# Kernel optimization log

Measured on AMD Instinct MI355X. Metric: run time of the kernel, lower is better.

Reference implementation:

```python
import jax, jax.numpy as jnp
import numpy as np

STATE_DIM = 128
NUM_STATES = 16
BATCH = 16384


def setup_inputs() -> dict:
    key = jax.random.key(0)
    k1, k2, k3, k4 = jax.random.split(key, 4)
    x = jax.random.normal(k1, (BATCH, STATE_DIM), dtype=jnp.float32)
    state_idx = jax.random.randint(k2, (BATCH,), 0, NUM_STATES)
    A_all = jax.random.normal(k3, (NUM_STATES, STATE_DIM, STATE_DIM), dtype=jnp.float32)
    C_all = jax.random.normal(k4, (NUM_STATES, STATE_DIM, STATE_DIM), dtype=jnp.float32)
    return {"x": x, "state_idx": state_idx, "A_all": A_all, "C_all": C_all}


def reference(x, state_idx, A_all, C_all):
    # Per-sample expert matrix gather: [B, D, D]
    Ag = A_all[state_idx]
    Cg = C_all[state_idx]
    # state = relu(x @ A_i) per sample, batched via einsum
    state = jax.nn.relu(jnp.einsum('bd,bde->be', x, Ag))
    # observation = state @ C_i
    out = jnp.einsum('be,bef->bf', state, Cg)
    return out
```

## Files before the change

### kernel.cpp

```cpp
#include <hip/hip_runtime.h>

#define D 128
#define NS 16
#define BATCH 16384
#define TILE 64
#define CHUNK 512
#define NCH (BATCH / CHUNK)

typedef __attribute__((ext_vector_type(8))) short short8;
typedef __attribute__((ext_vector_type(4))) float f32x4;

__device__ __forceinline__ unsigned short f2bf(float f) {
  unsigned u = __builtin_bit_cast(unsigned, f);
  u += 0x7FFFu + ((u >> 16) & 1u);
  return (unsigned short)(u >> 16);
}

__global__ __launch_bounds__(256, 2) void ssm_fused(
    const float* __restrict__ x,
    const int* __restrict__ sidx,
    const float* __restrict__ A_all,
    const float* __restrict__ C_all,
    float* __restrict__ out) {
  __shared__ __align__(16) char smemW[D * 136 * 2];
  unsigned short (*Ws)[136] = (unsigned short (*)[136])smemW;
  float (*T)[129] = (float (*)[129])smemW;
  __shared__ unsigned short Xs[TILE][136];
  __shared__ unsigned short Hs[TILE][136];
  __shared__ int rowlist[CHUNK];
  __shared__ int wcnt[8];

  const int s = blockIdx.y;
  const int c0 = blockIdx.x * CHUNK;
  const int tid = threadIdx.x;
  const int lane = tid & 63, w = tid >> 6;
  const int l15 = lane & 15, quad = lane >> 4;
  const int wr = w & 1, wc = w >> 1;

  const int v0 = sidx[c0 + tid];
  const int v1 = sidx[c0 + 256 + tid];
  const unsigned long long lanelt = (1ull << lane) - 1ull;
  const unsigned long long m0 = __ballot(v0 == s);
  const unsigned long long m1 = __ballot(v1 == s);
  if (lane == 0) { wcnt[w] = (int)__popcll(m0); wcnt[4 + w] = (int)__popcll(m1); }
  __syncthreads();
  int pre0 = 0, pre1 = 0, tot0 = 0, cnt = 0;
#pragma unroll
  for (int ww = 0; ww < 4; ww++) {
    if (ww < w) { pre0 += wcnt[ww]; pre1 += wcnt[4 + ww]; }
    tot0 += wcnt[ww];
    cnt += wcnt[ww] + wcnt[4 + ww];
  }
  if (v0 == s) rowlist[pre0 + (int)__popcll(m0 & lanelt)] = c0 + tid;
  if (v1 == s) rowlist[tot0 + pre1 + (int)__popcll(m1 & lanelt)] = c0 + 256 + tid;
  if (cnt == 0) return;

  uint4 atr[8], ctr[8];
  {
    const float* __restrict__ srcA = A_all + (size_t)s * D * D;
    const float* __restrict__ srcC = C_all + (size_t)s * D * D;
    const int ecol = (tid & 7) * 4;
    const int drow = tid >> 3;
#pragma unroll
    for (int mat = 0; mat < 2; mat++) {
      const float* __restrict__ src = mat ? srcC : srcA;
#pragma unroll
      for (int sl = 0; sl < 4; sl++) {
        const int e0 = sl * 32;
        __syncthreads();
#pragma unroll
        for (int i = 0; i < 4; i++) {
          const int d = drow + 32 * i;
          const float4 v = *(const float4*)(src + (size_t)d * D + e0 + ecol);
          T[ecol + 0][d] = v.x;
          T[ecol + 1][d] = v.y;
          T[ecol + 2][d] = v.z;
          T[ecol + 3][d] = v.w;
        }
        __syncthreads();
#pragma unroll
        for (int ii = 0; ii < 2; ii++) {
          const int c = (2 * sl + ii) * 256 + tid;
          const int e = (c >> 4) - e0;
          const int d0 = (c & 15) * 8;
          unsigned short p[8];
#pragma unroll
          for (int k = 0; k < 8; k++) p[k] = f2bf(T[e][d0 + k]);
          if (mat) ctr[2 * sl + ii] = *(const uint4*)p;
          else     atr[2 * sl + ii] = *(const uint4*)p;
        }
      }
    }
    __syncthreads();
  }

#pragma unroll 1
  for (int i0 = 0; i0 < cnt; i0 += TILE) {
    if (i0) __syncthreads();

#pragma unroll
    for (int i = 0; i < 8; i++) {
      const int c = i * 256 + tid;
      *(uint4*)&Ws[c >> 4][(c & 15) * 8] = atr[i];
    }
    {
      const int r = tid >> 2, q = tid & 3;
      const int rid = (i0 + r < cnt) ? rowlist[i0 + r] : -1;
      unsigned short* xr = &Xs[r][q * 32];
      if (rid >= 0) {
        const float4* src = (const float4*)(x + (size_t)rid * D + q * 32);
#pragma unroll
        for (int i = 0; i < 8; i++) {
          float4 v = src[i];
          ushort4 p;
          p.x = f2bf(v.x); p.y = f2bf(v.y); p.z = f2bf(v.z); p.w = f2bf(v.w);
          *(ushort4*)(xr + i * 4) = p;
        }
      } else {
        ushort4 z; z.x = z.y = z.z = z.w = 0;
#pragma unroll
        for (int i = 0; i < 8; i++) *(ushort4*)(xr + i * 4) = z;
      }
    }
    __syncthreads();

    f32x4 acc[2][4];
#pragma unroll
    for (int ti = 0; ti < 2; ti++)
#pragma unroll
      for (int nb = 0; nb < 4; nb++) acc[ti][nb] = (f32x4){0.f, 0.f, 0.f, 0.f};
#pragma unroll
    for (int kb = 0; kb < 4; kb++) {
      short8 aF0 = *(const short8*)&Xs[(wr * 2 + 0) * 16 + l15][kb * 32 + quad * 8];
      short8 aF1 = *(const short8*)&Xs[(wr * 2 + 1) * 16 + l15][kb * 32 + quad * 8];
#pragma unroll
      for (int nb = 0; nb < 4; nb++) {
        short8 bF = *(const short8*)&Ws[wc * 64 + nb * 16 + l15][kb * 32 + quad * 8];
        acc[0][nb] = __builtin_amdgcn_mfma_f32_16x16x32_bf16(aF0, bF, acc[0][nb], 0, 0, 0);
        acc[1][nb] = __builtin_amdgcn_mfma_f32_16x16x32_bf16(aF1, bF, acc[1][nb], 0, 0, 0);
      }
    }
#pragma unroll
    for (int ti = 0; ti < 2; ti++)
#pragma unroll
      for (int nb = 0; nb < 4; nb++)
#pragma unroll
        for (int rr = 0; rr < 4; rr++) {
          float v = acc[ti][nb][rr];
          Hs[(wr * 2 + ti) * 16 + quad * 4 + rr][wc * 64 + nb * 16 + l15] =
              f2bf(v > 0.f ? v : 0.f);
        }
    __syncthreads();

#pragma unroll
    for (int i = 0; i < 8; i++) {
      const int c = i * 256 + tid;
      *(uint4*)&Ws[c >> 4][(c & 15) * 8] = ctr[i];
    }
    __syncthreads();

#pragma unroll
    for (int ti = 0; ti < 2; ti++)
#pragma unroll
      for (int nb = 0; nb < 4; nb++) acc[ti][nb] = (f32x4){0.f, 0.f, 0.f, 0.f};
#pragma unroll
    for (int kb = 0; kb < 4; kb++) {
      short8 aF0 = *(const short8*)&Hs[(wr * 2 + 0) * 16 + l15][kb * 32 + quad * 8];
      short8 aF1 = *(const short8*)&Hs[(wr * 2 + 1) * 16 + l15][kb * 32 + quad * 8];
#pragma unroll
      for (int nb = 0; nb < 4; nb++) {
        short8 bF = *(const short8*)&Ws[wc * 64 + nb * 16 + l15][kb * 32 + quad * 8];
        acc[0][nb] = __builtin_amdgcn_mfma_f32_16x16x32_bf16(aF0, bF, acc[0][nb], 0, 0, 0);
        acc[1][nb] = __builtin_amdgcn_mfma_f32_16x16x32_bf16(aF1, bF, acc[1][nb], 0, 0, 0);
      }
    }

#pragma unroll
    for (int ti = 0; ti < 2; ti++)
#pragma unroll
      for (int rr = 0; rr < 4; rr++) {
        const int rl = (wr * 2 + ti) * 16 + quad * 4 + rr;
        if (i0 + rl < cnt) {
          float* orow = out + (size_t)rowlist[i0 + rl] * D + wc * 64 + l15;
#pragma unroll
          for (int nb = 0; nb < 4; nb++) orow[nb * 16] = acc[ti][nb][rr];
        }
      }
  }
}

extern "C" void kernel_launch(void* const* d_in, const int* in_sizes, int n_in,
                              void* d_out, int out_size, void* d_ws, size_t ws_size,
                              hipStream_t stream) {
  const float* x = (const float*)d_in[0];
  const int* sidx = (const int*)d_in[1];
  const float* A_all = (const float*)d_in[2];
  const float* C_all = (const float*)d_in[3];
  float* out = (float*)d_out;

  ssm_fused<<<dim3(NCH, NS), 256, 0, stream>>>(x, sidx, A_all, C_all, out);
}
```

Baseline: 79.16 us.

## Load weights row-major and gather B fragments with strided LDS reads

```diff
diff --git a/kernel.cpp b/kernel.cpp
--- a/kernel.cpp
+++ b/kernel.cpp
@@ -5,7 +5,7 @@
 #define BATCH 16384
 #define TILE 64
 #define CHUNK 512
-#define NCH (BATCH / CHUNK)
+#define WP 130
 
 typedef __attribute__((ext_vector_type(8))) short short8;
 typedef __attribute__((ext_vector_type(4))) float f32x4;
@@ -16,22 +16,27 @@
   return (unsigned short)(u >> 16);
 }
 
+__device__ __forceinline__ uint4 pack8(float4 a, float4 b) {
+  unsigned short p[8];
+  p[0] = f2bf(a.x); p[1] = f2bf(a.y); p[2] = f2bf(a.z); p[3] = f2bf(a.w);
+  p[4] = f2bf(b.x); p[5] = f2bf(b.y); p[6] = f2bf(b.z); p[7] = f2bf(b.w);
+  return *(const uint4*)p;
+}
+
 __global__ __launch_bounds__(256, 2) void ssm_fused(
     const float* __restrict__ x,
     const int* __restrict__ sidx,
     const float* __restrict__ A_all,
     const float* __restrict__ C_all,
     float* __restrict__ out) {
-  __shared__ __align__(16) char smemW[D * 136 * 2];
-  unsigned short (*Ws)[136] = (unsigned short (*)[136])smemW;
-  float (*T)[129] = (float (*)[129])smemW;
-  __shared__ unsigned short Xs[TILE][136];
-  __shared__ unsigned short Hs[TILE][136];
+  __shared__ unsigned short Ws[D * WP];
+  __shared__ unsigned short XH[TILE][136];
   __shared__ int rowlist[CHUNK];
   __shared__ int wcnt[8];
 
-  const int s = blockIdx.y;
-  const int c0 = blockIdx.x * CHUNK;
+  const int b = blockIdx.x;
+  const int s = (b & 7) | (((b >> 3) & 1) << 3);
+  const int c0 = (b >> 4) * CHUNK;
   const int tid = threadIdx.x;
   const int lane = tid & 63, w = tid >> 6;
   const int l15 = lane & 15, quad = lane >> 4;
@@ -39,6 +44,23 @@
 
   const int v0 = sidx[c0 + tid];
   const int v1 = sidx[c0 + 256 + tid];
+
+  uint4 atr[8], ctr[8];
+  {
+    const float* __restrict__ gA = A_all + (size_t)s * D * D;
+    const float* __restrict__ gC = C_all + (size_t)s * D * D;
+#pragma unroll
+    for (int i = 0; i < 8; i++) {
+      const int c = i * 256 + tid;
+      float4 a0 = *(const float4*)(gA + (size_t)c * 8);
+      float4 a1 = *(const float4*)(gA + (size_t)c * 8 + 4);
+      float4 e0 = *(const float4*)(gC + (size_t)c * 8);
+      float4 e1 = *(const float4*)(gC + (size_t)c * 8 + 4);
+      atr[i] = pack8(a0, a1);
+      ctr[i] = pack8(e0, e1);
+    }
+  }
+
   const unsigned long long lanelt = (1ull << lane) - 1ull;
   const unsigned long long m0 = __ballot(v0 == s);
   const unsigned long long m1 = __ballot(v1 == s);
@@ -55,71 +77,34 @@
   if (v1 == s) rowlist[tot0 + pre1 + (int)__popcll(m1 & lanelt)] = c0 + 256 + tid;
   if (cnt == 0) return;
 
-  uint4 atr[8], ctr[8];
-  {
-    const float* __restrict__ srcA = A_all + (size_t)s * D * D;
-    const float* __restrict__ srcC = C_all + (size_t)s * D * D;
-    const int ecol = (tid & 7) * 4;
-    const int drow = tid >> 3;
-#pragma unroll
-    for (int mat = 0; mat < 2; mat++) {
-      const float* __restrict__ src = mat ? srcC : srcA;
-#pragma unroll
-      for (int sl = 0; sl < 4; sl++) {
-        const int e0 = sl * 32;
-        __syncthreads();
-#pragma unroll
-        for (int i = 0; i < 4; i++) {
-          const int d = drow + 32 * i;
-          const float4 v = *(const float4*)(src + (size_t)d * D + e0 + ecol);
-          T[ecol + 0][d] = v.x;
-          T[ecol + 1][d] = v.y;
-          T[ecol + 2][d] = v.z;
-          T[ecol + 3][d] = v.w;
-        }
-        __syncthreads();
-#pragma unroll
-        for (int ii = 0; ii < 2; ii++) {
-          const int c = (2 * sl + ii) * 256 + tid;
-          const int e = (c >> 4) - e0;
-          const int d0 = (c & 15) * 8;
-          unsigned short p[8];
-#pragma unroll
-          for (int k = 0; k < 8; k++) p[k] = f2bf(T[e][d0 + k]);
-          if (mat) ctr[2 * sl + ii] = *(const uint4*)p;
-          else     atr[2 * sl + ii] = *(const uint4*)p;
-        }
-      }
-    }
-    __syncthreads();
-  }
-
 #pragma unroll 1
   for (int i0 = 0; i0 < cnt; i0 += TILE) {
-    if (i0) __syncthreads();
+    __syncthreads();
 
 #pragma unroll
     for (int i = 0; i < 8; i++) {
       const int c = i * 256 + tid;
-      *(uint4*)&Ws[c >> 4][(c & 15) * 8] = atr[i];
+      const int base = (c >> 4) * WP + (c & 15) * 8;
+      const unsigned* pw = (const unsigned*)&atr[i];
+#pragma unroll
+      for (int k = 0; k < 4; k++) *(unsigned*)&Ws[base + k * 2] = pw[k];
     }
     {
       const int r = tid >> 2, q = tid & 3;
       const int rid = (i0 + r < cnt) ? rowlist[i0 + r] : -1;
-      unsigned short* xr = &Xs[r][q * 32];
+      unsigned short* xr = &XH[r][q * 32];
       if (rid >= 0) {
         const float4* src = (const float4*)(x + (size_t)rid * D + q * 32);
 #pragma unroll
-        for (int i = 0; i < 8; i++) {
-          float4 v = src[i];
-          ushort4 p;
-          p.x = f2bf(v.x); p.y = f2bf(v.y); p.z = f2bf(v.z); p.w = f2bf(v.w);
-          *(ushort4*)(xr + i * 4) = p;
+        for (int i = 0; i < 4; i++) {
+          float4 va = src[2 * i];
+          float4 vb = src[2 * i + 1];
+          *(uint4*)(xr + i * 8) = pack8(va, vb);
         }
       } else {
-        ushort4 z; z.x = z.y = z.z = z.w = 0;
+        uint4 z = {0, 0, 0, 0};
 #pragma unroll
-        for (int i = 0; i < 8; i++) *(ushort4*)(xr + i * 4) = z;
+        for (int i = 0; i < 4; i++) *(uint4*)(xr + i * 8) = z;
       }
     }
     __syncthreads();
@@ -131,15 +116,21 @@
       for (int nb = 0; nb < 4; nb++) acc[ti][nb] = (f32x4){0.f, 0.f, 0.f, 0.f};
 #pragma unroll
     for (int kb = 0; kb < 4; kb++) {
-      short8 aF0 = *(const short8*)&Xs[(wr * 2 + 0) * 16 + l15][kb * 32 + quad * 8];
-      short8 aF1 = *(const short8*)&Xs[(wr * 2 + 1) * 16 + l15][kb * 32 + quad * 8];
+      short8 aF0 = *(const short8*)&XH[(wr * 2 + 0) * 16 + l15][kb * 32 + quad * 8];
+      short8 aF1 = *(const short8*)&XH[(wr * 2 + 1) * 16 + l15][kb * 32 + quad * 8];
+      const int rbase = (kb * 32 + quad * 8) * WP;
 #pragma unroll
       for (int nb = 0; nb < 4; nb++) {
-        short8 bF = *(const short8*)&Ws[wc * 64 + nb * 16 + l15][kb * 32 + quad * 8];
+        const int col = wc * 64 + nb * 16 + l15;
+        short8 bF;
+#pragma unroll
+        for (int j = 0; j < 8; j++) bF[j] = (short)Ws[rbase + j * WP + col];
         acc[0][nb] = __builtin_amdgcn_mfma_f32_16x16x32_bf16(aF0, bF, acc[0][nb], 0, 0, 0);
         acc[1][nb] = __builtin_amdgcn_mfma_f32_16x16x32_bf16(aF1, bF, acc[1][nb], 0, 0, 0);
       }
     }
+    __syncthreads();
+
 #pragma unroll
     for (int ti = 0; ti < 2; ti++)
 #pragma unroll
@@ -147,15 +138,16 @@
 #pragma unroll
         for (int rr = 0; rr < 4; rr++) {
           float v = acc[ti][nb][rr];
-          Hs[(wr * 2 + ti) * 16 + quad * 4 + rr][wc * 64 + nb * 16 + l15] =
+          XH[(wr * 2 + ti) * 16 + quad * 4 + rr][wc * 64 + nb * 16 + l15] =
               f2bf(v > 0.f ? v : 0.f);
         }
-    __syncthreads();
-
 #pragma unroll
     for (int i = 0; i < 8; i++) {
       const int c = i * 256 + tid;
-      *(uint4*)&Ws[c >> 4][(c & 15) * 8] = ctr[i];
+      const int base = (c >> 4) * WP + (c & 15) * 8;
+      const unsigned* pw = (const unsigned*)&ctr[i];
+#pragma unroll
+      for (int k = 0; k < 4; k++) *(unsigned*)&Ws[base + k * 2] = pw[k];
     }
     __syncthreads();
 
@@ -165,11 +157,15 @@
       for (int nb = 0; nb < 4; nb++) acc[ti][nb] = (f32x4){0.f, 0.f, 0.f, 0.f};
 #pragma unroll
     for (int kb = 0; kb < 4; kb++) {
-      short8 aF0 = *(const short8*)&Hs[(wr * 2 + 0) * 16 + l15][kb * 32 + quad * 8];
-      short8 aF1 = *(const short8*)&Hs[(wr * 2 + 1) * 16 + l15][kb * 32 + quad * 8];
+      short8 aF0 = *(const short8*)&XH[(wr * 2 + 0) * 16 + l15][kb * 32 + quad * 8];
+      short8 aF1 = *(const short8*)&XH[(wr * 2 + 1) * 16 + l15][kb * 32 + quad * 8];
+      const int rbase = (kb * 32 + quad * 8) * WP;
 #pragma unroll
       for (int nb = 0; nb < 4; nb++) {
-        short8 bF = *(const short8*)&Ws[wc * 64 + nb * 16 + l15][kb * 32 + quad * 8];
+        const int col = wc * 64 + nb * 16 + l15;
+        short8 bF;
+#pragma unroll
+        for (int j = 0; j < 8; j++) bF[j] = (short)Ws[rbase + j * WP + col];
         acc[0][nb] = __builtin_amdgcn_mfma_f32_16x16x32_bf16(aF0, bF, acc[0][nb], 0, 0, 0);
         acc[1][nb] = __builtin_amdgcn_mfma_f32_16x16x32_bf16(aF1, bF, acc[1][nb], 0, 0, 0);
       }
@@ -198,5 +194,5 @@
   const float* C_all = (const float*)d_in[3];
   float* out = (float*)d_out;
 
-  ssm_fused<<<dim3(NCH, NS), 256, 0, stream>>>(x, sidx, A_all, C_all, out);
+  ssm_fused<<<512, 256, 0, stream>>>(x, sidx, A_all, C_all, out);
 }
```

New measurement: 73.96 us. -6.6%, faster.
